# Kernel optimization log

Measured on AMD Instinct MI355X. Metric: run time of the kernel, lower is better.

## Reference

```python
import jax, jax.numpy as jnp
import numpy as np

B, C, H, W = 32, 384, 32, 32
NH = 4            # num_heads
CC = 192          # conv_channels = ceil(384/2)
HID = 1536        # mlp hidden = 4*dim
EPS = 1e-6


def _ln2d(x, w, b):
    # LayerNorm over channel axis of NCHW
    u = x.mean(1, keepdims=True)
    s = ((x - u) ** 2).mean(1, keepdims=True)
    return w[:, None, None] * ((x - u) * jax.lax.rsqrt(s + EPS)) + b[:, None, None]


def setup_inputs() -> dict:
    key = jax.random.key(0)
    ks = jax.random.split(key, 8)
    f = lambda k, shp, sc: jax.random.normal(k, shp, jnp.float32) * sc
    return {
        "x": f(ks[0], (B, C, H, W), 1.0),
        "conv_w": f(ks[1], (CC, 1, 3, 3), 0.1),
        "conv_b": jnp.zeros((CC,), jnp.float32),
        "nxca_w": jnp.ones((C,), jnp.float32),
        "nxca_b": jnp.zeros((C,), jnp.float32),
        "temp": jnp.ones((NH, 1, 1), jnp.float32),
        "qkv_w": f(ks[2], (3 * C, C), 0.05),
        "qkv_b": jnp.zeros((3 * C,), jnp.float32),
        "proj_w": f(ks[3], (C, C), 0.05),
        "proj_b": jnp.zeros((C,), jnp.float32),
        "norm_w": jnp.ones((C,), jnp.float32),
        "norm_b": jnp.zeros((C,), jnp.float32),
        "fc1_w": f(ks[4], (HID, C), 0.05),
        "fc1_b": jnp.zeros((HID,), jnp.float32),
        "fc2_w": f(ks[5], (C, HID), 0.05),
        "fc2_b": jnp.zeros((C,), jnp.float32),
        "gamma_xca": jnp.ones((C,), jnp.float32),
        "gamma": jnp.ones((C,), jnp.float32),
    }


def reference(x, conv_w, conv_b, nxca_w, nxca_b, temp, qkv_w, qkv_b,
              proj_w, proj_b, norm_w, norm_b, fc1_w, fc1_b, fc2_w, fc2_b,
              gamma_xca, gamma):
    b, c, h, w = x.shape
    n = h * w
    hd = c // NH
    # depthwise 3x3 conv on first CC channels (in-place in torch -> shortcut
    # taken AFTER the conv, faithfully reproduced here)
    xc = jax.lax.conv_general_dilated(
        x[:, :CC], conv_w, (1, 1), ((1, 1), (1, 1)), feature_group_count=CC
    ) + conv_b[None, :, None, None]
    x = jnp.concatenate([xc, x[:, CC:]], axis=1)
    shortcut = x
    # XCA branch
    y = _ln2d(x, nxca_w, nxca_b)
    yf = y.reshape(b, c, n).transpose(0, 2, 1)                       # [B,N,C]
    qkv = (yf @ qkv_w.T + qkv_b).reshape(b, n, 3, NH, hd).transpose(2, 0, 3, 1, 4)
    q, k, v = qkv[0], qkv[1], qkv[2]                                  # [B,h,N,hd]
    q = q / jnp.maximum(jnp.linalg.norm(q, axis=-1, keepdims=True), 1e-12)
    k = k / jnp.maximum(jnp.linalg.norm(k, axis=-1, keepdims=True), 1e-12)
    attn = jax.nn.softmax(jnp.einsum('bhnd,bhmd->bhnm', q, k) * temp, axis=-1)
    o = jnp.einsum('bhnm,bhmd->bhnd', attn, v).transpose(0, 2, 1, 3).reshape(b, n, c)
    o = (o @ proj_w.T + proj_b).transpose(0, 2, 1).reshape(b, c, h, w)
    x = shortcut + gamma_xca[None, :, None, None] * o
    # MLP branch
    shortcut2 = x
    z = _ln2d(x, norm_w, norm_b).transpose(0, 2, 3, 1).reshape(b, n, c)
    z = jax.nn.gelu(z @ fc1_w.T + fc1_b, approximate=False) @ fc2_w.T + fc2_b
    z = z.reshape(b, h, w, c).transpose(0, 3, 1, 2)
    return shortcut2 + gamma[None, :, None, None] * z
```

## Files before the change

kernel.cpp:

```cpp
#include <hip/hip_runtime.h>
#include <cstdint>

typedef unsigned short u16;
typedef unsigned int u32;
typedef unsigned long long u64;
typedef __attribute__((ext_vector_type(4))) float f32x4;
typedef __attribute__((ext_vector_type(8))) __bf16 bf16x8;
typedef __attribute__((ext_vector_type(8))) u16 u16x8;

#define DEV __device__ __forceinline__

DEV u16 f2bf(float f) {
  u32 u = __builtin_bit_cast(u32, f);
  u += 0x7fffu + ((u >> 16) & 1u);
  return (u16)(u >> 16);
}
DEV float bflo2f(u32 packed) { return __builtin_bit_cast(float, packed << 16); }
DEV float bfhi2f(u32 packed) { return __builtin_bit_cast(float, packed & 0xffff0000u); }

DEV void g2l16(void* lds_wave_base, const void* gsrc) {
  __builtin_amdgcn_global_load_lds(
      (const __attribute__((address_space(1))) u32*)gsrc,
      (__attribute__((address_space(3))) u32*)lds_wave_base, 16, 0, 0);
}

__global__ __launch_bounds__(256) void conv_k(const float* __restrict__ x,
                                              const float* __restrict__ cw,
                                              const float* __restrict__ cb,
                                              float* __restrict__ xc) {
  int id = blockIdx.x * 256 + threadIdx.x;
  int p = id & 1023;
  int bc = id >> 10;
  int c = bc % 384;
  float v;
  if (c < 192) {
    int hh = p >> 5, ww = p & 31;
    float a = cb[c];
    const float* xp = x + ((size_t)bc << 10);
    const float* wp = cw + c * 9;
#pragma unroll
    for (int dy = 0; dy < 3; ++dy) {
      int y = hh + dy - 1;
      if ((unsigned)y < 32u) {
#pragma unroll
        for (int dx = 0; dx < 3; ++dx) {
          int xw = ww + dx - 1;
          if ((unsigned)xw < 32u) a += xp[y * 32 + xw] * wp[dy * 3 + dx];
        }
      }
    }
    v = a;
  } else {
    v = x[id];
  }
  xc[id] = v;
}

__global__ __launch_bounds__(256) void cvt_k(const float* __restrict__ in,
                                             u16* __restrict__ out, int n) {
  int id = blockIdx.x * 256 + threadIdx.x;
  if (id < n) out[id] = f2bf(in[id]);
}

__global__ __launch_bounds__(256) void ln_t_k(const float* __restrict__ X,
                                              const float* __restrict__ w,
                                              const float* __restrict__ bsh,
                                              u16* __restrict__ Y) {
  __shared__ float tile[384][33];
  __shared__ float ps[8][32], ps2[8][32];
  __shared__ float mean_s[32], rstd_s[32];
  const int b = blockIdx.y;
  const int p0 = blockIdx.x * 32;
  const int t = threadIdx.x;
  const int pl = t & 31, cg = t >> 5;
  const float* xb = X + (((size_t)b * 384) << 10) + p0 + pl;
  float s = 0.f, s2 = 0.f;
  for (int c = cg; c < 384; c += 8) {
    float v = xb[(size_t)c << 10];
    tile[c][pl] = v;
    s += v;
    s2 += v * v;
  }
  ps[cg][pl] = s;
  ps2[cg][pl] = s2;
  __syncthreads();
  if (t < 32) {
    float a = 0.f, a2 = 0.f;
#pragma unroll
    for (int g = 0; g < 8; ++g) { a += ps[g][t]; a2 += ps2[g][t]; }
    float mu = a * (1.f / 384.f);
    float var = a2 * (1.f / 384.f) - mu * mu;
    mean_s[t] = mu;
    rstd_s[t] = rsqrtf(var + 1e-6f);
  }
  __syncthreads();
  const int cl = t & 63, pg = t >> 6;
  for (int p = pg; p < 32; p += 4) {
    float mu = mean_s[p], rs = rstd_s[p];
    size_t orow = (((size_t)b << 10) + p0 + p) * 384;
#pragma unroll
    for (int cc = 0; cc < 6; ++cc) {
      int c = cc * 64 + cl;
      float v = (tile[c][p] - mu) * rs * w[c] + bsh[c];
      Y[orow + c] = f2bf(v);
    }
  }
}

__global__ __launch_bounds__(256) void normqk_k(u16* __restrict__ Qn,
                                                u16* __restrict__ Kn,
                                                const float* __restrict__ temp) {
  const int t = threadIdx.x;
  const int w = t >> 6, l = t & 63;
  const int rg = l >> 4, li = l & 15;
  const int row = blockIdx.x * 16 + w * 4 + rg;
  const float tmp = temp[(row >> 10) & 3];
#pragma unroll
  for (int arr = 0; arr < 2; ++arr) {
    u16* p = arr ? (Kn + (size_t)row * 128 + li * 6)
                 : (Qn + (size_t)row * 96 + li * 6);
    u32 a = *(const u32*)p;
    u32 b2 = *(const u32*)(p + 2);
    u32 c = *(const u32*)(p + 4);
    float v[6] = {bflo2f(a), bfhi2f(a), bflo2f(b2), bfhi2f(b2), bflo2f(c), bfhi2f(c)};
    float ss = 0.f;
#pragma unroll
    for (int i = 0; i < 6; ++i) ss += v[i] * v[i];
#pragma unroll
    for (int mk = 1; mk < 16; mk <<= 1) ss += __shfl_xor(ss, mk, 64);
    float sc = 1.0f / fmaxf(sqrtf(ss), 1e-12f);
    if (arr == 0) sc *= tmp;
    u32 o0 = (u32)f2bf(v[0] * sc) | ((u32)f2bf(v[1] * sc) << 16);
    u32 o1 = (u32)f2bf(v[2] * sc) | ((u32)f2bf(v[3] * sc) << 16);
    u32 o2 = (u32)f2bf(v[4] * sc) | ((u32)f2bf(v[5] * sc) << 16);
    *(u32*)p = o0;
    *(u32*)(p + 2) = o1;
    *(u32*)(p + 4) = o2;
  }
}

__global__ __launch_bounds__(256) void attn_k(const u16* __restrict__ Qn,
                                              const u16* __restrict__ Kg,
                                              const u16* __restrict__ Vg,
                                              u16* __restrict__ O,
                                              const float* __restrict__ temp) {
  __shared__ u16 Kt[2][8192];
  __shared__ u16 Vt[2][6144];
  __shared__ u16 Pt[4][2304];
  const int t = threadIdx.x;
  const int w = t >> 6, l = t & 63;
  const int l15 = l & 15, kg = l >> 4;
  const int id = blockIdx.x;
  const int xcd = id & 7, jj = id >> 3;
  const int bh = xcd * 16 + (jj >> 3);
  const int qb = jj & 7;
  const int b = bh >> 2, h = bh & 3;
  const int q0 = qb * 128 + w * 32;
  const u16* Qb = Qn + (size_t)bh * 98304;
  const u16* Kbg = Kg + (size_t)bh * 131072;
  const u16* Vbg = Vg + (size_t)bh * 98304;
  const float T = fabsf(temp[h]);

  u32 sK[4], sV[3];
#pragma unroll
  for (int j = 0; j < 4; ++j) {
    u32 s = w * 4096 + j * 1024 + l * 16;
    sK[j] = s ^ (((s >> 8) & 7) << 4);
  }
#pragma unroll
  for (int j = 0; j < 3; ++j) {
    u32 s = w * 3072 + j * 1024 + l * 16;
    u32 u = s ^ (((s >> 7) & 7) << 4);
    sV[j] = (u >> 7) * 2048 + (u & 127);
  }
  u32 cs[3];
#pragma unroll
  for (int kk = 0; kk < 3; ++kk)
    cs[kk] = (u32)((kk * 64 + kg * 16) ^ ((l15 & 7) << 4));

  bf16x8 qf[2][3];
#pragma unroll
  for (int f = 0; f < 2; ++f) {
    const u16* qp = Qb + (size_t)(q0 + f * 16 + l15) * 96 + kg * 8;
#pragma unroll
    for (int kk = 0; kk < 3; ++kk) qf[f][kk] = *(const bf16x8*)(qp + kk * 32);
  }
  f32x4 oa[2][6];
#pragma unroll
  for (int f = 0; f < 2; ++f)
#pragma unroll
    for (int d = 0; d < 6; ++d) oa[f][d] = {0.f, 0.f, 0.f, 0.f};
  float l_r[2][4] = {{0.f, 0.f, 0.f, 0.f}, {0.f, 0.f, 0.f, 0.f}};
  __bf16* Pw = (__bf16*)&Pt[w][0];

#define STAGE(buf, kv0)                                                        \
  {                                                                            \
    const char* kb = (const char*)Kbg + (size_t)(kv0) * 256;                   \
    const char* vb = (const char*)Vbg + (size_t)(kv0) * 2;                     \
    char* kd = (char*)&Kt[buf][0] + w * 4096;                                  \
    char* vd = (char*)&Vt[buf][0] + w * 3072;                                  \
    g2l16(kd, kb + sK[0]);                                                     \
    g2l16(kd + 1024, kb + sK[1]);                                              \
    g2l16(kd + 2048, kb + sK[2]);                                              \
    g2l16(kd + 3072, kb + sK[3]);                                              \
    g2l16(vd, vb + sV[0]);                                                     \
    g2l16(vd + 1024, vb + sV[1]);                                              \
    g2l16(vd + 2048, vb + sV[2]);                                              \
  }

  STAGE(0, 0);
  for (int tt = 0; tt < 16; ++tt) {
    const int cur = tt & 1;
    if (tt < 15) {
      STAGE(cur ^ 1, (tt + 1) * 64);
      asm volatile("s_waitcnt vmcnt(7)" ::: "memory");
    } else {
      asm volatile("s_waitcnt vmcnt(0)" ::: "memory");
    }
    __builtin_amdgcn_s_barrier();
    const char* Kc = (const char*)&Kt[cur][0];
    const char* Vc = (const char*)&Vt[cur][0];
    f32x4 s0[4], s1[4];
#pragma unroll
    for (int n = 0; n < 4; ++n) { s0[n] = {0.f, 0.f, 0.f, 0.f}; s1[n] = {0.f, 0.f, 0.f, 0.f}; }
#pragma unroll
    for (int n = 0; n < 4; ++n) {
      const char* krow = Kc + ((n * 16 + l15) << 8);
#pragma unroll
      for (int kk = 0; kk < 3; ++kk) {
        bf16x8 kf = *(const bf16x8*)(krow + cs[kk]);
        s0[n] = __builtin_amdgcn_mfma_f32_16x16x32_bf16(qf[0][kk], kf, s0[n], 0, 0, 0);
        s1[n] = __builtin_amdgcn_mfma_f32_16x16x32_bf16(qf[1][kk], kf, s1[n], 0, 0, 0);
      }
    }
#pragma unroll
    for (int n = 0; n < 4; ++n) {
#pragma unroll
      for (int j = 0; j < 4; ++j) {
        float p0 = __expf(s0[n][j] - T);
        float p1 = __expf(s1[n][j] - T);
        l_r[0][j] += p0;
        l_r[1][j] += p1;
        Pw[(kg * 4 + j) * 72 + n * 16 + l15] = (__bf16)p0;
        Pw[(16 + kg * 4 + j) * 72 + n * 16 + l15] = (__bf16)p1;
      }
    }
#pragma unroll
    for (int kk = 0; kk < 2; ++kk) {
      bf16x8 pf0 = *(const bf16x8*)(Pw + (size_t)l15 * 72 + kk * 32 + kg * 8);
      bf16x8 pf1 = *(const bf16x8*)(Pw + (size_t)(16 + l15) * 72 + kk * 32 + kg * 8);
#pragma unroll
      for (int d = 0; d < 6; ++d) {
        bf16x8 vf = *(const bf16x8*)(Vc + ((d * 16 + l15) << 7) + cs[kk]);
        oa[0][d] = __builtin_amdgcn_mfma_f32_16x16x32_bf16(pf0, vf, oa[0][d], 0, 0, 0);
        oa[1][d] = __builtin_amdgcn_mfma_f32_16x16x32_bf16(pf1, vf, oa[1][d], 0, 0, 0);
      }
    }
    __builtin_amdgcn_s_barrier();
  }
#undef STAGE
  float inv[2][4];
#pragma unroll
  for (int f = 0; f < 2; ++f)
#pragma unroll
    for (int j = 0; j < 4; ++j) {
      float sum = l_r[f][j];
#pragma unroll
      for (int mk = 1; mk < 16; mk <<= 1) sum += __shfl_xor(sum, mk, 64);
      inv[f][j] = 1.0f / sum;
    }
#pragma unroll
  for (int f = 0; f < 2; ++f)
#pragma unroll
    for (int d = 0; d < 6; ++d)
#pragma unroll
      for (int j = 0; j < 4; ++j) {
        int tok = q0 + f * 16 + kg * 4 + j;
        O[((size_t)b * 1024 + tok) * 384 + h * 96 + d * 16 + l15] =
            f2bf(oa[f][d][j] * inv[f][j]);
      }
}

template <int EPI, bool SWZ>
__global__ __launch_bounds__(256) void gemm_k(const u16* __restrict__ A,
                                              const u16* __restrict__ B, int M,
                                              int N, int K,
                                              const float* __restrict__ bias,
                                              const float* gamma,
                                              const float* res, void* outp,
                                              int nbx) {
  __shared__ u16 At[128 * 32];
  __shared__ u16 Bt[128 * 32];
  const int t = threadIdx.x;
  const int w = t >> 6, l = t & 63;
  const int l15 = l & 15, kg = l >> 4;
  int bx, by;
  if (SWZ) {
    int id = blockIdx.x;
    int xcd = id & 7, jj = id >> 3;
    int q = jj / nbx;
    bx = jj - q * nbx;
    by = xcd * 32 + q;
  } else {
    bx = blockIdx.x; by = blockIdx.y;
  }
  const int m0 = by * 128, n0 = bx * 128;
  const int wr = w >> 1, wc = w & 1;

  const int off1 = w * 1024 + l * 16;
  const int off2 = 4096 + w * 1024 + l * 16;
  const int r1 = off1 >> 6, c1 = off1 & 63;
  const int r2 = off2 >> 6, c2 = off2 & 63;
  const size_t ldab = (size_t)K * 2;
  const char* pa1 = (const char*)A + (size_t)(m0 + r1) * ldab + c1;
  const char* pa2 = (const char*)A + (size_t)(m0 + r2) * ldab + c2;
  const char* pb1 = (const char*)B + (size_t)(n0 + r1) * ldab + c1;
  const char* pb2 = (const char*)B + (size_t)(n0 + r2) * ldab + c2;
  char* At1 = (char*)At + w * 1024;
  char* At2 = (char*)At + 4096 + w * 1024;
  char* Bt1 = (char*)Bt + w * 1024;
  char* Bt2 = (char*)Bt + 4096 + w * 1024;

  f32x4 acc[4][4];
#pragma unroll
  for (int m = 0; m < 4; ++m)
#pragma unroll
    for (int n = 0; n < 4; ++n) acc[m][n] = {0.f, 0.f, 0.f, 0.f};

  const int nkt = K >> 5;
  for (int kt = 0; kt < nkt; ++kt) {
    g2l16(At1, pa1);
    g2l16(At2, pa2);
    g2l16(Bt1, pb1);
    g2l16(Bt2, pb2);
    pa1 += 64; pa2 += 64; pb1 += 64; pb2 += 64;
    __syncthreads();
    bf16x8 af[4], bfr[4];
#pragma unroll
    for (int m = 0; m < 4; ++m)
      af[m] = *(const bf16x8*)(At + (wr * 64 + m * 16 + l15) * 32 + kg * 8);
#pragma unroll
    for (int n = 0; n < 4; ++n)
      bfr[n] = *(const bf16x8*)(Bt + (wc * 64 + n * 16 + l15) * 32 + kg * 8);
#pragma unroll
    for (int m = 0; m < 4; ++m)
#pragma unroll
      for (int n = 0; n < 4; ++n)
        acc[m][n] = __builtin_amdgcn_mfma_f32_16x16x32_bf16(af[m], bfr[n], acc[m][n], 0, 0, 0);
    __syncthreads();
  }

  if (EPI == 1) {
    u16* out = (u16*)outp;
#pragma unroll
    for (int m = 0; m < 4; ++m) {
#pragma unroll
      for (int n = 0; n < 4; ++n) {
        int gcol = n0 + wc * 64 + n * 16 + l15;
        float bs = bias[gcol];
#pragma unroll
        for (int j = 0; j < 4; ++j) {
          int grow = m0 + wr * 64 + m * 16 + kg * 4 + j;
          float v = acc[m][n][j] + bs;
          v = 0.5f * v * (1.0f + erff(v * 0.70710678118f));
          out[(size_t)grow * N + gcol] = f2bf(v);
        }
      }
    }
  } else if (EPI == 2) {
    float* out = (float*)outp;
#pragma unroll
    for (int m = 0; m < 4; ++m) {
#pragma unroll
      for (int n = 0; n < 4; ++n) {
        int tok = n0 + wc * 64 + n * 16 + l15;
        int bb = tok >> 10, p = tok & 1023;
#pragma unroll
        for (int j = 0; j < 4; ++j) {
          int c = m0 + wr * 64 + m * 16 + kg * 4 + j;
          size_t addr = (((size_t)(bb * 384 + c)) << 10) + p;
          out[addr] = res[addr] + gamma[c] * (acc[m][n][j] + bias[c]);
        }
      }
    }
  } else {
    u16* Qp = (u16*)outp;
    u16* Kp = Qp + 12582912;
    u16* Vp = Kp + 16777216;
    const int sec = n0 / 384;
#pragma unroll
    for (int m = 0; m < 4; ++m) {
      const int tokbase = m0 + wr * 64 + m * 16 + kg * 4;
      const int bb = tokbase >> 10, nb = tokbase & 1023;
#pragma unroll
      for (int n = 0; n < 4; ++n) {
        int gcol = n0 + wc * 64 + n * 16 + l15;
        int within = gcol - sec * 384;
        int hh = within / 96;
        int dd = within - hh * 96;
        float bs = bias[gcol];
        int bh = bb * 4 + hh;
        if (sec == 0) {
          u16* ptr = Qp + ((size_t)bh * 1024 + nb) * 96 + dd;
#pragma unroll
          for (int j = 0; j < 4; ++j) ptr[(size_t)j * 96] = f2bf(acc[m][n][j] + bs);
        } else if (sec == 1) {
          u16* ptr = Kp + (((size_t)bh * 1024 + nb) << 7) + dd;
#pragma unroll
          for (int j = 0; j < 4; ++j) ptr[(size_t)j << 7] = f2bf(acc[m][n][j] + bs);
        } else {
          u64 pk = 0;
#pragma unroll
          for (int j = 0; j < 4; ++j)
            pk |= (u64)f2bf(acc[m][n][j] + bs) << (16 * j);
          *(u64*)(Vp + ((size_t)bh * 96 + dd) * 1024 + nb) = pk;
        }
      }
    }
  }
}

extern "C" void kernel_launch(void* const* d_in, const int* in_sizes, int n_in,
                              void* d_out, int out_size, void* d_ws,
                              size_t ws_size, hipStream_t stream) {
  const float* x      = (const float*)d_in[0];
  const float* conv_w = (const float*)d_in[1];
  const float* conv_b = (const float*)d_in[2];
  const float* nxca_w = (const float*)d_in[3];
  const float* nxca_b = (const float*)d_in[4];
  const float* temp   = (const float*)d_in[5];
  const float* qkv_w  = (const float*)d_in[6];
  const float* qkv_b  = (const float*)d_in[7];
  const float* proj_w = (const float*)d_in[8];
  const float* proj_b = (const float*)d_in[9];
  const float* norm_w = (const float*)d_in[10];
  const float* norm_b = (const float*)d_in[11];
  const float* fc1_w  = (const float*)d_in[12];
  const float* fc1_b  = (const float*)d_in[13];
  const float* fc2_w  = (const float*)d_in[14];
  const float* fc2_b  = (const float*)d_in[15];
  const float* g_xca  = (const float*)d_in[16];
  const float* g_mlp  = (const float*)d_in[17];
  (void)in_sizes; (void)n_in; (void)out_size; (void)ws_size;

  char* ws = (char*)d_ws;
  float* xc  = (float*)(ws);
  u16* Y     = (u16*)(ws + 50331648);
  u16* Qn    = (u16*)(ws + 75497472);
  u16* Kn    = (u16*)(ws + 100663296);
  u16* Vt    = (u16*)(ws + 134217728);
  u16* Obuf  = Y;
  u16* H1    = Qn;
  u16* wq    = (u16*)(ws + 176160768);
  u16* wp    = (u16*)(ws + 177045504);
  u16* w1    = (u16*)(ws + 177340416);
  u16* w2    = (u16*)(ws + 178520064);

  cvt_k<<<1728, 256, 0, stream>>>(qkv_w, wq, 442368);
  cvt_k<<<576, 256, 0, stream>>>(proj_w, wp, 147456);
  cvt_k<<<2304, 256, 0, stream>>>(fc1_w, w1, 589824);
  cvt_k<<<2304, 256, 0, stream>>>(fc2_w, w2, 589824);

  conv_k<<<49152, 256, 0, stream>>>(x, conv_w, conv_b, xc);
  ln_t_k<<<dim3(32, 32), 256, 0, stream>>>(xc, nxca_w, nxca_b, Y);
  gemm_k<3, true><<<2304, 256, 0, stream>>>(Y, wq, 32768, 1152, 384, qkv_b,
                                            nullptr, nullptr, Qn, 9);
  normqk_k<<<8192, 256, 0, stream>>>(Qn, Kn, temp);
  attn_k<<<1024, 256, 0, stream>>>(Qn, Kn, Vt, Obuf, temp);
  gemm_k<2, false><<<dim3(256, 3), 256, 0, stream>>>(wp, Obuf, 384, 32768, 384,
                                                     proj_b, g_xca, xc, xc, 0);
  ln_t_k<<<dim3(32, 32), 256, 0, stream>>>(xc, norm_w, norm_b, Y);
  gemm_k<1, true><<<3072, 256, 0, stream>>>(Y, w1, 32768, 1536, 384, fc1_b,
                                            nullptr, nullptr, H1, 12);
  gemm_k<2, false><<<dim3(256, 3), 256, 0, stream>>>(w2, H1, 384, 32768, 1536,
                                                     fc2_b, g_mlp, xc,
                                                     (float*)d_out, 0);
}
```

Before: 486.1 us.

## Double-buffer GEMM LDS tiles, stage epilogue stores through LDS, use tanh GELU

The GEMM kernel now double-buffers its A/B tiles in one shared LDS array, so the next k-tile's global-to-LDS load is issued before the MFMAs on the current tile, with one barrier per iteration. The bf16 epilogues for the Q/K and fc1 outputs are first written into LDS and then stored as 16-byte rows, replacing scattered 2-byte stores. The erf-based GELU is replaced by a tanh approximation built on __expf, and the hand-written rounding is replaced by a native bf16 conversion. The proj and fc2 GEMMs switch to a 1-D grid with an XCD-aware block mapping. The tanh GELU introduces small numerical differences from the exact-erf reference.

```diff
diff --git a/kernel.cpp b/kernel.cpp
--- a/kernel.cpp
+++ b/kernel.cpp
@@ -10,6 +10,10 @@
 
 #define DEV __device__ __forceinline__
 
+DEV u16 cvt16(float f) {
+  __bf16 h = (__bf16)f;
+  return __builtin_bit_cast(u16, h);
+}
 DEV u16 f2bf(float f) {
   u32 u = __builtin_bit_cast(u32, f);
   u += 0x7fffu + ((u >> 16) & 1u);
@@ -22,6 +26,13 @@
   __builtin_amdgcn_global_load_lds(
       (const __attribute__((address_space(1))) u32*)gsrc,
       (__attribute__((address_space(3))) u32*)lds_wave_base, 16, 0, 0);
+}
+
+DEV float gelu_tanh(float v) {
+  float z = v * (0.7978845608f + 0.0356774081f * v * v);
+  float e = __expf(2.0f * z);
+  float th = 1.0f - 2.0f / (e + 1.0f);
+  return 0.5f * v * (1.0f + th);
 }
 
 __global__ __launch_bounds__(256) void conv_k(const float* __restrict__ x,
@@ -281,7 +292,7 @@
       }
 }
 
-template <int EPI, bool SWZ>
+template <int EPI, int SWZ>
 __global__ __launch_bounds__(256) void gemm_k(const u16* __restrict__ A,
                                               const u16* __restrict__ B, int M,
                                               int N, int K,
@@ -289,18 +300,22 @@
                                               const float* gamma,
                                               const float* res, void* outp,
                                               int nbx) {
-  __shared__ u16 At[128 * 32];
-  __shared__ u16 Bt[128 * 32];
+  __shared__ u16 SM[16384];
   const int t = threadIdx.x;
   const int w = t >> 6, l = t & 63;
   const int l15 = l & 15, kg = l >> 4;
   int bx, by;
-  if (SWZ) {
+  if (SWZ == 1) {
     int id = blockIdx.x;
     int xcd = id & 7, jj = id >> 3;
     int q = jj / nbx;
     bx = jj - q * nbx;
     by = xcd * 32 + q;
+  } else if (SWZ == 2) {
+    int id = blockIdx.x;
+    int xcd = id & 7, jj = id >> 3;
+    by = jj % 3;
+    bx = (jj / 3) * 8 + xcd;
   } else {
     bx = blockIdx.x; by = blockIdx.y;
   }
@@ -316,10 +331,7 @@
   const char* pa2 = (const char*)A + (size_t)(m0 + r2) * ldab + c2;
   const char* pb1 = (const char*)B + (size_t)(n0 + r1) * ldab + c1;
   const char* pb2 = (const char*)B + (size_t)(n0 + r2) * ldab + c2;
-  char* At1 = (char*)At + w * 1024;
-  char* At2 = (char*)At + 4096 + w * 1024;
-  char* Bt1 = (char*)Bt + w * 1024;
-  char* Bt2 = (char*)Bt + 4096 + w * 1024;
+  char* SMc = (char*)SM;
 
   f32x4 acc[4][4];
 #pragma unroll
@@ -328,20 +340,31 @@
     for (int n = 0; n < 4; ++n) acc[m][n] = {0.f, 0.f, 0.f, 0.f};
 
   const int nkt = K >> 5;
+  {
+    char* ad = SMc + w * 1024;
+    char* bd = SMc + 16384 + w * 1024;
+    g2l16(ad, pa1); g2l16(ad + 4096, pa2);
+    g2l16(bd, pb1); g2l16(bd + 4096, pb2);
+  }
+  __syncthreads();
   for (int kt = 0; kt < nkt; ++kt) {
-    g2l16(At1, pa1);
-    g2l16(At2, pa2);
-    g2l16(Bt1, pb1);
-    g2l16(Bt2, pb2);
-    pa1 += 64; pa2 += 64; pb1 += 64; pb2 += 64;
-    __syncthreads();
+    const int buf = kt & 1;
+    if (kt + 1 < nkt) {
+      const size_t o = (size_t)(kt + 1) * 64;
+      char* ad = SMc + (buf ^ 1) * 8192 + w * 1024;
+      char* bd = SMc + 16384 + (buf ^ 1) * 8192 + w * 1024;
+      g2l16(ad, pa1 + o); g2l16(ad + 4096, pa2 + o);
+      g2l16(bd, pb1 + o); g2l16(bd + 4096, pb2 + o);
+    }
+    const u16* Ab = SM + buf * 4096;
+    const u16* Bb = SM + 8192 + buf * 4096;
     bf16x8 af[4], bfr[4];
 #pragma unroll
     for (int m = 0; m < 4; ++m)
-      af[m] = *(const bf16x8*)(At + (wr * 64 + m * 16 + l15) * 32 + kg * 8);
+      af[m] = *(const bf16x8*)(Ab + (wr * 64 + m * 16 + l15) * 32 + kg * 8);
 #pragma unroll
     for (int n = 0; n < 4; ++n)
-      bfr[n] = *(const bf16x8*)(Bt + (wc * 64 + n * 16 + l15) * 32 + kg * 8);
+      bfr[n] = *(const bf16x8*)(Bb + (wc * 64 + n * 16 + l15) * 32 + kg * 8);
 #pragma unroll
     for (int m = 0; m < 4; ++m)
 #pragma unroll
@@ -350,24 +373,7 @@
     __syncthreads();
   }
 
-  if (EPI == 1) {
-    u16* out = (u16*)outp;
-#pragma unroll
-    for (int m = 0; m < 4; ++m) {
-#pragma unroll
-      for (int n = 0; n < 4; ++n) {
-        int gcol = n0 + wc * 64 + n * 16 + l15;
-        float bs = bias[gcol];
-#pragma unroll
-        for (int j = 0; j < 4; ++j) {
-          int grow = m0 + wr * 64 + m * 16 + kg * 4 + j;
-          float v = acc[m][n][j] + bs;
-          v = 0.5f * v * (1.0f + erff(v * 0.70710678118f));
-          out[(size_t)grow * N + gcol] = f2bf(v);
-        }
-      }
-    }
-  } else if (EPI == 2) {
+  if (EPI == 2) {
     float* out = (float*)outp;
 #pragma unroll
     for (int m = 0; m < 4; ++m) {
@@ -383,38 +389,79 @@
         }
       }
     }
-  } else {
-    u16* Qp = (u16*)outp;
-    u16* Kp = Qp + 12582912;
-    u16* Vp = Kp + 16777216;
-    const int sec = n0 / 384;
+    return;
+  }
+
+  const int sec = (EPI == 3) ? (n0 / 384) : 0;
+  if (EPI == 3 && sec == 2) {
+    u16* Vp = (u16*)outp + 12582912 + 16777216;
 #pragma unroll
     for (int m = 0; m < 4; ++m) {
       const int tokbase = m0 + wr * 64 + m * 16 + kg * 4;
       const int bb = tokbase >> 10, nb = tokbase & 1023;
 #pragma unroll
       for (int n = 0; n < 4; ++n) {
-        int gcol = n0 + wc * 64 + n * 16 + l15;
-        int within = gcol - sec * 384;
+        int within = n0 - 768 + wc * 64 + n * 16 + l15;
         int hh = within / 96;
         int dd = within - hh * 96;
-        float bs = bias[gcol];
+        float bs = bias[768 + within];
         int bh = bb * 4 + hh;
-        if (sec == 0) {
-          u16* ptr = Qp + ((size_t)bh * 1024 + nb) * 96 + dd;
-#pragma unroll
-          for (int j = 0; j < 4; ++j) ptr[(size_t)j * 96] = f2bf(acc[m][n][j] + bs);
-        } else if (sec == 1) {
-          u16* ptr = Kp + (((size_t)bh * 1024 + nb) << 7) + dd;
-#pragma unroll
-          for (int j = 0; j < 4; ++j) ptr[(size_t)j << 7] = f2bf(acc[m][n][j] + bs);
-        } else {
-          u64 pk = 0;
-#pragma unroll
-          for (int j = 0; j < 4; ++j)
-            pk |= (u64)f2bf(acc[m][n][j] + bs) << (16 * j);
-          *(u64*)(Vp + ((size_t)bh * 96 + dd) * 1024 + nb) = pk;
+        u64 pk = 0;
+#pragma unroll
+        for (int j = 0; j < 4; ++j)
+          pk |= (u64)cvt16(acc[m][n][j] + bs) << (16 * j);
+        *(u64*)(Vp + ((size_t)bh * 96 + dd) * 1024 + nb) = pk;
+      }
+    }
+    return;
+  }
+
+  {
+    u16* Ct = SM;
+    float bs[4];
+#pragma unroll
+    for (int n = 0; n < 4; ++n) bs[n] = bias[n0 + wc * 64 + n * 16 + l15];
+    u16* cw_ = Ct + (wr * 64 + kg * 4) * 128 + wc * 64 + l15;
+#pragma unroll
+    for (int m = 0; m < 4; ++m)
+#pragma unroll
+      for (int n = 0; n < 4; ++n)
+#pragma unroll
+        for (int j = 0; j < 4; ++j) {
+          float v = acc[m][n][j] + bs[n];
+          if (EPI == 1) v = gelu_tanh(v);
+          cw_[(m * 16 + j) * 128 + n * 16] = cvt16(v);
         }
+    __syncthreads();
+    const int row_l = w * 4 + (l >> 4);
+    const int colc = (l & 15) * 8;
+    const u16* src = Ct + row_l * 128 + colc;
+    if (EPI == 1) {
+      u16* dst = (u16*)outp + (size_t)(m0 + row_l) * N + n0 + colc;
+#pragma unroll
+      for (int rr = 0; rr < 8; ++rr)
+        *(u16x8*)(dst + (size_t)rr * 16 * N) =
+            *(const u16x8*)(src + rr * 16 * 128);
+    } else {
+      int within = n0 - sec * 384 + colc;
+      int hh = within / 96;
+      int dd = within - hh * 96;
+      int tokb = m0 + row_l;
+      int bb = tokb >> 10, nb = tokb & 1023;
+      int bh = bb * 4 + hh;
+      u16* dp;
+      int stride;
+      if (sec == 0) {
+        dp = (u16*)outp + ((size_t)bh * 1024 + nb) * 96 + dd;
+        stride = 16 * 96;
+      } else {
+        dp = (u16*)outp + 12582912 + (((size_t)bh * 1024 + nb) << 7) + dd;
+        stride = 16 * 128;
+      }
+#pragma unroll
+      for (int rr = 0; rr < 8; ++rr) {
+        *(u16x8*)dp = *(const u16x8*)(src + rr * 16 * 128);
+        dp += stride;
       }
     }
   }
@@ -463,16 +510,15 @@
 
   conv_k<<<49152, 256, 0, stream>>>(x, conv_w, conv_b, xc);
   ln_t_k<<<dim3(32, 32), 256, 0, stream>>>(xc, nxca_w, nxca_b, Y);
-  gemm_k<3, true><<<2304, 256, 0, stream>>>(Y, wq, 32768, 1152, 384, qkv_b,
-                                            nullptr, nullptr, Qn, 9);
+  gemm_k<3, 1><<<2304, 256, 0, stream>>>(Y, wq, 32768, 1152, 384, qkv_b,
+                                         nullptr, nullptr, Qn, 9);
   normqk_k<<<8192, 256, 0, stream>>>(Qn, Kn, temp);
   attn_k<<<1024, 256, 0, stream>>>(Qn, Kn, Vt, Obuf, temp);
-  gemm_k<2, false><<<dim3(256, 3), 256, 0, stream>>>(wp, Obuf, 384, 32768, 384,
-                                                     proj_b, g_xca, xc, xc, 0);
+  gemm_k<2, 2><<<768, 256, 0, stream>>>(wp, Obuf, 384, 32768, 384,
+                                        proj_b, g_xca, xc, xc, 0);
   ln_t_k<<<dim3(32, 32), 256, 0, stream>>>(xc, norm_w, norm_b, Y);
-  gemm_k<1, true><<<3072, 256, 0, stream>>>(Y, w1, 32768, 1536, 384, fc1_b,
-                                            nullptr, nullptr, H1, 12);
-  gemm_k<2, false><<<dim3(256, 3), 256, 0, stream>>>(w2, H1, 384, 32768, 1536,
-                                                     fc2_b, g_mlp, xc,
-                                                     (float*)d_out, 0);
-}
+  gemm_k<1, 1><<<3072, 256, 0, stream>>>(Y, w1, 32768, 1536, 384, fc1_b,
+                                         nullptr, nullptr, H1, 12);
+  gemm_k<2, 2><<<768, 256, 0, stream>>>(w2, H1, 384, 32768, 1536,
+                                        fc2_b, g_mlp, xc, (float*)d_out, 0);
+}
```

Result: faster. 453.9 us (-6.6%).
